# Performance work log

Hardware: AMD Instinct MI355X
Metric: run time of the kernel (lower is better)

The kernel has to match this reference:

```python
import jax, jax.numpy as jnp
import numpy as np


def _gather_nbrs(feats, idx):
    # feats: [C, N], idx: [N, k] -> [C, N, k]
    return feats[:, idx]


def pointconv_dw(xyz, feats, idx, w_pos, b_pos, w_out, b_out):
    """Depthwise point conv: per-channel weights from relative neighbor coords.
    xyz: [B,3,N], feats: [B,C,N], idx: [B,N,k] -> [B,C_out,N]
    """
    nbr_xyz = jax.vmap(_gather_nbrs)(xyz, idx)            # [B,3,N,k]
    rel = nbr_xyz - xyz[:, :, :, None]                    # relative positions
    w = jnp.einsum('cd,bdnk->bcnk', w_pos, rel) + b_pos[None, :, None, None]
    g = jax.vmap(_gather_nbrs)(feats, idx)                # [B,C,N,k]
    agg = jnp.sum(w * g, axis=-1)                         # [B,C,N] depthwise reduce over k
    return jnp.einsum('oc,bcn->bon', w_out, agg) + b_out[None, :, None]


def setup_inputs() -> dict:
    key = jax.random.key(0)
    ks = jax.random.split(key, 16)
    B, N, K = 2, 65536, 4
    IN, HID = 64, 64
    C = HID + IN
    s = 0.02
    inp = {
        'xyz': jax.random.normal(ks[0], (B, 3, N), jnp.float32),
        'h': jax.random.normal(ks[1], (B, HID, N), jnp.float32),
        'x': jax.random.normal(ks[2], (B, IN, N), jnp.float32),
        'knn_indices': jax.random.randint(ks[3], (B, N, K), 0, N, jnp.int32),
    }
    names = ['z', 'r', 'q']
    for i, nm in enumerate(names):
        inp[f'w{nm}_pos'] = s * jax.random.normal(ks[4 + 4 * i], (C, 3), jnp.float32)
        inp[f'b{nm}_pos'] = jnp.zeros((C,), jnp.float32)
        inp[f'w{nm}_out'] = s * jax.random.normal(ks[5 + 4 * i], (HID, C), jnp.float32)
        inp[f'b{nm}_out'] = jnp.zeros((HID,), jnp.float32)
    return inp


def reference(xyz, h, x, knn_indices,
              wz_pos, bz_pos, wz_out, bz_out,
              wr_pos, br_pos, wr_out, br_out,
              wq_pos, bq_pos, wq_out, bq_out):
    hx = jnp.concatenate([h, x], axis=1)                  # [B, HID+IN, N]
    z = jax.nn.sigmoid(pointconv_dw(xyz, hx, knn_indices, wz_pos, bz_pos, wz_out, bz_out))
    r = jax.nn.sigmoid(pointconv_dw(xyz, hx, knn_indices, wr_pos, br_pos, wr_out, br_out))
    rhx = jnp.concatenate([r * h, x], axis=1)
    q = jnp.tanh(pointconv_dw(xyz, rhx, knn_indices, wq_pos, bq_pos, wq_out, bq_out))
    return (1.0 - z) * h + z * q
```

## Files before the change

### kernel.cpp

```cpp
#include <hip/hip_runtime.h>

#define NPTS 65536
#define BATCH 2
#define CCH 128
#define HIDC 64
#define PPB 32
#define LDB 520
#define PLD 136

typedef unsigned short u16;
typedef unsigned int u32;
typedef __bf16 bf16_t;
typedef bf16_t bf16x8 __attribute__((ext_vector_type(8)));
typedef float f32x4 __attribute__((ext_vector_type(4)));

__device__ __forceinline__ u16 f2bf(float f){
  union { float f; unsigned u; } v; v.f = f;
  unsigned r = v.u + 0x7FFFu + ((v.u >> 16) & 1u);
  return (u16)(r >> 16);
}
__device__ __forceinline__ float bf2f(u16 u){
  union { unsigned u; float f; } v; v.u = ((unsigned)u) << 16; return v.f;
}
__device__ __forceinline__ u32 pkrn(float a, float b){
  union { float f; u32 u; } ua, ub; ua.f = a; ub.f = b;
  return ((ua.u + 0x8000u) >> 16) | ((ub.u + 0x8000u) & 0xffff0000u);
}
__device__ __forceinline__ float sigmoidf_(float v){ return 1.f/(1.f+__expf(-v)); }
__device__ __forceinline__ float tanhf_(float v){
  v = fminf(10.f, fmaxf(-10.f, v));
  float e = __expf(2.f*v);
  return (e-1.f)/(e+1.f);
}

__global__ __launch_bounds__(256) void kprep(
    const float* __restrict__ wz, const float* __restrict__ wzp, const float* __restrict__ bzp,
    const float* __restrict__ wr, const float* __restrict__ wrp, const float* __restrict__ brp,
    const float* __restrict__ wq, const float* __restrict__ wqp, const float* __restrict__ bqp,
    u16* __restrict__ A){
  int idx = blockIdx.x*256 + threadIdx.x;
  int t = idx & 7, o = (idx>>3)&63, quad = (idx>>9)&3, s = (idx>>11)&15, g = idx>>15;
  int pk = s*32 + quad*8 + t;
  int j = pk>>7, chunk = (pk>>3)&15, tt = pk&7;
  int orig = chunk*32 + j*8 + tt;
  int c = orig>>2, m = orig&3;
  const float* W  = (g==0)? wz  : (g==1)? wr  : wq;
  const float* wp = (g==0)? wzp : (g==1)? wrp : wqp;
  const float* bp = (g==0)? bzp : (g==1)? brp : bqp;
  float coef = m ? wp[c*3 + m - 1] : bp[c];
  A[idx] = f2bf(W[o*CCH + c] * coef);
}

__global__ __launch_bounds__(256) void k_pack(const float* __restrict__ h,
    const float* __restrict__ x, u16* __restrict__ hxT, u16* __restrict__ rhxT){
  __shared__ __align__(16) u16 tile[64*PLD];
  int tid = threadIdx.x;
  int b = blockIdx.x >> 10, n0 = (blockIdx.x & 1023) << 6;
  #pragma unroll
  for (int i = 0; i < 8; ++i){
    int cc = (tid>>4) + i*16;
    int nn = (tid & 15)*4;
    const float* src = (cc < HIDC)
        ? (h + (((size_t)(b*HIDC + cc))<<16) + n0 + nn)
        : (x + (((size_t)(b*HIDC + cc - HIDC))<<16) + n0 + nn);
    float4 v = *(const float4*)src;
    tile[(nn+0)*PLD + cc] = f2bf(v.x);
    tile[(nn+1)*PLD + cc] = f2bf(v.y);
    tile[(nn+2)*PLD + cc] = f2bf(v.z);
    tile[(nn+3)*PLD + cc] = f2bf(v.w);
  }
  __syncthreads();
  #pragma unroll
  for (int i = 0; i < 4; ++i){
    int tsk = tid + (i<<8);
    int n = tsk>>4, ch = (tsk&15)*8;
    uint4 v = *(const uint4*)(tile + n*PLD + ch);
    *(uint4*)(hxT + (((size_t)(b<<16) + n0 + n)<<7) + ch) = v;
  }
  #pragma unroll
  for (int i = 0; i < 2; ++i){
    int tsk = tid + (i<<8);
    int n = tsk>>3, ch = HIDC + (tsk&7)*8;
    uint4 v = *(const uint4*)(tile + n*PLD + ch);
    *(uint4*)(rhxT + (((size_t)(b<<16) + n0 + n)<<7) + ch) = v;
  }
}

#define ACCUM(gv, rv) { \
  u32 dw_[4] = {gv.x, gv.y, gv.z, gv.w}; \
  _Pragma("unroll") \
  for (int q_ = 0; q_ < 4; ++q_){ \
    union { u32 u; float f; } lo_, hi_; \
    lo_.u = dw_[q_] << 16; hi_.u = dw_[q_] & 0xffff0000u; \
    m0[2*q_]   += lo_.f; mx[2*q_]   += rv.x*lo_.f; my[2*q_]   += rv.y*lo_.f; mz[2*q_]   += rv.z*lo_.f; \
    m0[2*q_+1] += hi_.f; mx[2*q_+1] += rv.x*hi_.f; my[2*q_+1] += rv.y*hi_.f; mz[2*q_+1] += rv.z*hi_.f; \
  } }

__global__ __launch_bounds__(256, 4) void k_zr(
    const float* __restrict__ xyz, const float* __restrict__ h,
    const int* __restrict__ knn,
    const float* __restrict__ bz_out, const float* __restrict__ br_out,
    const u16* __restrict__ Azr,
    const u16* __restrict__ hxT, u16* __restrict__ rhxT, u16* __restrict__ z_ws)
{
  __shared__ __align__(16) u16 bext[PPB*LDB];
  __shared__ __align__(16) float4 relk[PPB*4];
  __shared__ __align__(16) int4 jlds[PPB];

  int tid = threadIdx.x; int lane = tid & 63; int wv = tid >> 6;
  int b = blockIdx.x >> 11, n0 = (blockIdx.x & 2047) << 5;
  size_t bN = (size_t)b * NPTS;

  if (tid < 128){
    int p = tid >> 2, k = tid & 3;
    int j = knn[((bN + n0 + p) << 2) + k];
    ((int*)jlds)[tid] = j;
    const float* xb = xyz + (size_t)b*3*NPTS;
    float cx = xb[n0+p], cy = xb[NPTS + n0+p], cz = xb[2*NPTS + n0+p];
    relk[tid] = make_float4(xb[j]-cx, xb[NPTS+j]-cy, xb[2*NPTS+j]-cz, 0.f);
  }
  __syncthreads();

  const u16* hxTb = hxT + (bN << 7);
  #pragma unroll
  for (int it = 0; it < 2; ++it){
    int task = tid + (it << 8);
    int p = task >> 4, chunk = task & 15;
    int4 jj = jlds[p];
    uint4 g0 = *(const uint4*)(hxTb + (((size_t)jj.x)<<7) + chunk*8);
    uint4 g1 = *(const uint4*)(hxTb + (((size_t)jj.y)<<7) + chunk*8);
    uint4 g2 = *(const uint4*)(hxTb + (((size_t)jj.z)<<7) + chunk*8);
    uint4 g3 = *(const uint4*)(hxTb + (((size_t)jj.w)<<7) + chunk*8);
    float4 r0 = relk[p*4+0], r1 = relk[p*4+1], r2 = relk[p*4+2], r3 = relk[p*4+3];
    float m0[8] = {0,0,0,0,0,0,0,0}, mx[8] = {0,0,0,0,0,0,0,0};
    float my[8] = {0,0,0,0,0,0,0,0}, mz[8] = {0,0,0,0,0,0,0,0};
    ACCUM(g0, r0); ACCUM(g1, r1); ACCUM(g2, r2); ACCUM(g3, r3);
    u16* row = bext + p*LDB;
    #pragma unroll
    for (int j = 0; j < 4; ++j){
      int ca = 2*j, cb = 2*j+1;
      uint4 v;
      v.x = pkrn(m0[ca], mx[ca]); v.y = pkrn(my[ca], mz[ca]);
      v.z = pkrn(m0[cb], mx[cb]); v.w = pkrn(my[cb], mz[cb]);
      *(uint4*)(row + j*128 + chunk*8) = v;
    }
  }
  __syncthreads();

  int l15 = lane & 15, quad = lane >> 4;
  int orow = wv*16 + l15;
  f32x4 accz[2], accr[2];
  #pragma unroll
  for (int nt = 0; nt < 2; ++nt){ accz[nt] = (f32x4){0,0,0,0}; accr[nt] = (f32x4){0,0,0,0}; }
  #pragma unroll
  for (int s = 0; s < 16; ++s){
    bf16x8 az = *(const bf16x8*)(Azr + ((s*4 + quad)*64 + orow)*8);
    bf16x8 ar = *(const bf16x8*)(Azr + 32768 + ((s*4 + quad)*64 + orow)*8);
    #pragma unroll
    for (int nt = 0; nt < 2; ++nt){
      bf16x8 bb = *(const bf16x8*)(bext + (nt*16 + l15)*LDB + s*32 + quad*8);
      accz[nt] = __builtin_amdgcn_mfma_f32_16x16x32_bf16(az, bb, accz[nt], 0, 0, 0);
      accr[nt] = __builtin_amdgcn_mfma_f32_16x16x32_bf16(ar, bb, accr[nt], 0, 0, 0);
    }
  }
  __syncthreads();

  u16* zst  = bext;
  u16* rhst = bext + 64*40;
  #pragma unroll
  for (int nt = 0; nt < 2; ++nt){
    #pragma unroll
    for (int reg = 0; reg < 4; ++reg){
      int o = wv*16 + quad*4 + reg;
      int p = nt*16 + l15;
      float zf = sigmoidf_(accz[nt][reg] + bz_out[o]);
      float rf = sigmoidf_(accr[nt][reg] + br_out[o]);
      float hv = h[(((size_t)(b*HIDC + o))<<16) + n0 + p];
      zst[o*40 + p] = f2bf(zf);
      rhst[p*72 + o] = f2bf(rf * hv);
    }
  }
  __syncthreads();

  {
    int p = tid >> 3, ch = (tid & 7)*8;
    uint4 v = *(const uint4*)(rhst + p*72 + ch);
    *(uint4*)(rhxT + ((bN + n0 + p)<<7) + ch) = v;
  }
  {
    int o = tid >> 2, pc = (tid & 3)*8;
    uint4 v = *(const uint4*)(zst + o*40 + pc);
    *(uint4*)(z_ws + (((size_t)(b*HIDC + o))<<16) + n0 + pc) = v;
  }
}

__global__ __launch_bounds__(256, 4) void k_q(
    const float* __restrict__ xyz, const float* __restrict__ h,
    const int* __restrict__ knn,
    const float* __restrict__ bq_out,
    const u16* __restrict__ Aq,
    const u16* __restrict__ rhxT, const u16* __restrict__ z_ws,
    float* __restrict__ out)
{
  __shared__ __align__(16) u16 bext[PPB*LDB];
  __shared__ __align__(16) float4 relk[PPB*4];
  __shared__ __align__(16) int4 jlds[PPB];

  int tid = threadIdx.x; int lane = tid & 63; int wv = tid >> 6;
  int b = blockIdx.x >> 11, n0 = (blockIdx.x & 2047) << 5;
  size_t bN = (size_t)b * NPTS;

  if (tid < 128){
    int p = tid >> 2, k = tid & 3;
    int j = knn[((bN + n0 + p) << 2) + k];
    ((int*)jlds)[tid] = j;
    const float* xb = xyz + (size_t)b*3*NPTS;
    float cx = xb[n0+p], cy = xb[NPTS + n0+p], cz = xb[2*NPTS + n0+p];
    relk[tid] = make_float4(xb[j]-cx, xb[NPTS+j]-cy, xb[2*NPTS+j]-cz, 0.f);
  }
  __syncthreads();

  const u16* rhxTb = rhxT + (bN << 7);
  #pragma unroll
  for (int it = 0; it < 2; ++it){
    int task = tid + (it << 8);
    int p = task >> 4, chunk = task & 15;
    int4 jj = jlds[p];
    uint4 g0 = *(const uint4*)(rhxTb + (((size_t)jj.x)<<7) + chunk*8);
    uint4 g1 = *(const uint4*)(rhxTb + (((size_t)jj.y)<<7) + chunk*8);
    uint4 g2 = *(const uint4*)(rhxTb + (((size_t)jj.z)<<7) + chunk*8);
    uint4 g3 = *(const uint4*)(rhxTb + (((size_t)jj.w)<<7) + chunk*8);
    float4 r0 = relk[p*4+0], r1 = relk[p*4+1], r2 = relk[p*4+2], r3 = relk[p*4+3];
    float m0[8] = {0,0,0,0,0,0,0,0}, mx[8] = {0,0,0,0,0,0,0,0};
    float my[8] = {0,0,0,0,0,0,0,0}, mz[8] = {0,0,0,0,0,0,0,0};
    ACCUM(g0, r0); ACCUM(g1, r1); ACCUM(g2, r2); ACCUM(g3, r3);
    u16* row = bext + p*LDB;
    #pragma unroll
    for (int j = 0; j < 4; ++j){
      int ca = 2*j, cb = 2*j+1;
      uint4 v;
      v.x = pkrn(m0[ca], mx[ca]); v.y = pkrn(my[ca], mz[ca]);
      v.z = pkrn(m0[cb], mx[cb]); v.w = pkrn(my[cb], mz[cb]);
      *(uint4*)(row + j*128 + chunk*8) = v;
    }
  }
  __syncthreads();

  int l15 = lane & 15, quad = lane >> 4;
  int orow = wv*16 + l15;
  f32x4 acc[2];
  #pragma unroll
  for (int nt = 0; nt < 2; ++nt) acc[nt] = (f32x4){0,0,0,0};
  #pragma unroll
  for (int s = 0; s < 16; ++s){
    bf16x8 aq = *(const bf16x8*)(Aq + ((s*4 + quad)*64 + orow)*8);
    #pragma unroll
    for (int nt = 0; nt < 2; ++nt){
      bf16x8 bb = *(const bf16x8*)(bext + (nt*16 + l15)*LDB + s*32 + quad*8);
      acc[nt] = __builtin_amdgcn_mfma_f32_16x16x32_bf16(aq, bb, acc[nt], 0, 0, 0);
    }
  }

  #pragma unroll
  for (int nt = 0; nt < 2; ++nt){
    #pragma unroll
    for (int reg = 0; reg < 4; ++reg){
      int o = wv*16 + quad*4 + reg;
      int p = nt*16 + l15;
      size_t idx = (((size_t)(b*HIDC + o))<<16) + n0 + p;
      float qf = tanhf_(acc[nt][reg] + bq_out[o]);
      float zf = bf2f(z_ws[idx]);
      float hv = h[idx];
      out[idx] = (1.f - zf)*hv + zf*qf;
    }
  }
}

extern "C" void kernel_launch(void* const* d_in, const int* in_sizes, int n_in,
                              void* d_out, int out_size, void* d_ws, size_t ws_size,
                              hipStream_t stream){
  const float* xyz    = (const float*)d_in[0];
  const float* h      = (const float*)d_in[1];
  const float* x      = (const float*)d_in[2];
  const int*   knn    = (const int*)d_in[3];
  const float* wz_pos = (const float*)d_in[4];
  const float* bz_pos = (const float*)d_in[5];
  const float* wz_out = (const float*)d_in[6];
  const float* bz_out = (const float*)d_in[7];
  const float* wr_pos = (const float*)d_in[8];
  const float* br_pos = (const float*)d_in[9];
  const float* wr_out = (const float*)d_in[10];
  const float* br_out = (const float*)d_in[11];
  const float* wq_pos = (const float*)d_in[12];
  const float* bq_pos = (const float*)d_in[13];
  const float* wq_out = (const float*)d_in[14];
  const float* bq_out = (const float*)d_in[15];
  float* out = (float*)d_out;

  u16* ws   = (u16*)d_ws;
  u16* hxT  = ws;
  u16* rhxT = hxT + (size_t)BATCH*NPTS*CCH;
  u16* z_ws = rhxT + (size_t)BATCH*NPTS*CCH;
  u16* A    = z_ws + (size_t)BATCH*HIDC*NPTS;

  kprep<<<384, 256, 0, stream>>>(wz_out, wz_pos, bz_pos, wr_out, wr_pos, br_pos,
                                 wq_out, wq_pos, bq_pos, A);
  k_pack<<<2048, 256, 0, stream>>>(h, x, hxT, rhxT);
  k_zr<<<4096, 256, 0, stream>>>(xyz, h, knn, bz_out, br_out, A, hxT, rhxT, z_ws);
  k_q<<<4096, 256, 0, stream>>>(xyz, h, knn, bq_out, A + 65536, rhxT, z_ws, out);
}
```

Baseline: 234.9 us.

## Split q conv into x-part computed in k_zr and gather only r*h in k_q

The q pointconv is linear in its input channels, so the contribution from the x channels (which do not depend on r) is computed inside k_zr using the already-gathered hx features and stored as a bf16 pre-activation. k_q then gathers only the 64 r*h channels from a narrower 64-channel buffer and processes 64 points per block. k_pack no longer writes x into a second buffer. This is meant to cut gather traffic and MFMA work in k_q, at the cost of extra MFMAs and an extra output stream in k_zr, plus bf16 rounding of the partial sum.

```diff
diff --git a/kernel.cpp b/kernel.cpp
--- a/kernel.cpp
+++ b/kernel.cpp
@@ -4,9 +4,9 @@
 #define BATCH 2
 #define CCH 128
 #define HIDC 64
-#define PPB 32
 #define LDB 520
-#define PLD 136
+#define LDB2 264
+#define PLD 130
 
 typedef unsigned short u16;
 typedef unsigned int u32;
@@ -39,20 +39,31 @@
     const float* __restrict__ wq, const float* __restrict__ wqp, const float* __restrict__ bqp,
     u16* __restrict__ A){
   int idx = blockIdx.x*256 + threadIdx.x;
-  int t = idx & 7, o = (idx>>3)&63, quad = (idx>>9)&3, s = (idx>>11)&15, g = idx>>15;
-  int pk = s*32 + quad*8 + t;
-  int j = pk>>7, chunk = (pk>>3)&15, tt = pk&7;
-  int orig = chunk*32 + j*8 + tt;
-  int c = orig>>2, m = orig&3;
-  const float* W  = (g==0)? wz  : (g==1)? wr  : wq;
-  const float* wp = (g==0)? wzp : (g==1)? wrp : wqp;
-  const float* bp = (g==0)? bzp : (g==1)? brp : bqp;
-  float coef = m ? wp[c*3 + m - 1] : bp[c];
-  A[idx] = f2bf(W[o*CCH + c] * coef);
+  if (idx < 98304){
+    int t = idx & 7, o = (idx>>3)&63, quad = (idx>>9)&3, s = (idx>>11)&15, g = idx>>15;
+    int pk = s*32 + quad*8 + t;
+    int j = pk>>7, chunk = (pk>>3)&15, tt = pk&7;
+    int orig = chunk*32 + j*8 + tt;
+    int c = orig>>2, m = orig&3;
+    const float* W  = (g==0)? wz  : (g==1)? wr  : wq;
+    const float* wp = (g==0)? wzp : (g==1)? wrp : wqp;
+    const float* bp = (g==0)? bzp : (g==1)? brp : bqp;
+    float coef = m ? wp[c*3 + m - 1] : bp[c];
+    A[idx] = f2bf(W[o*CCH + c] * coef);
+  } else {
+    int i2 = idx - 98304;
+    int t = i2 & 7, o = (i2>>3)&63, quad = (i2>>9)&3, s = (i2>>11)&7;
+    int k2 = s*32 + quad*8 + t;
+    int j = k2>>6, chunk = (k2>>3)&7, tt = k2&7;
+    int orig = chunk*32 + j*8 + tt;
+    int c = orig>>2, m = orig&3;
+    float coef = m ? wqp[c*3 + m - 1] : bqp[c];
+    A[idx] = f2bf(wq[o*CCH + c] * coef);
+  }
 }
 
 __global__ __launch_bounds__(256) void k_pack(const float* __restrict__ h,
-    const float* __restrict__ x, u16* __restrict__ hxT, u16* __restrict__ rhxT){
+    const float* __restrict__ x, u16* __restrict__ hxT){
   __shared__ __align__(16) u16 tile[64*PLD];
   int tid = threadIdx.x;
   int b = blockIdx.x >> 10, n0 = (blockIdx.x & 1023) << 6;
@@ -77,13 +88,6 @@
     uint4 v = *(const uint4*)(tile + n*PLD + ch);
     *(uint4*)(hxT + (((size_t)(b<<16) + n0 + n)<<7) + ch) = v;
   }
-  #pragma unroll
-  for (int i = 0; i < 2; ++i){
-    int tsk = tid + (i<<8);
-    int n = tsk>>3, ch = HIDC + (tsk&7)*8;
-    uint4 v = *(const uint4*)(tile + n*PLD + ch);
-    *(uint4*)(rhxT + (((size_t)(b<<16) + n0 + n)<<7) + ch) = v;
-  }
 }
 
 #define ACCUM(gv, rv) { \
@@ -96,16 +100,27 @@
     m0[2*q_+1] += hi_.f; mx[2*q_+1] += rv.x*hi_.f; my[2*q_+1] += rv.y*hi_.f; mz[2*q_+1] += rv.z*hi_.f; \
   } }
 
+#define PACKROW(row, CHOFF, STRIDE) { \
+  _Pragma("unroll") \
+  for (int j_ = 0; j_ < 4; ++j_){ \
+    int ca_ = 2*j_, cb_ = 2*j_+1; \
+    uint4 v_; \
+    v_.x = pkrn(m0[ca_], mx[ca_]); v_.y = pkrn(my[ca_], mz[ca_]); \
+    v_.z = pkrn(m0[cb_], mx[cb_]); v_.w = pkrn(my[cb_], mz[cb_]); \
+    *(uint4*)((row) + j_*(STRIDE) + (CHOFF)) = v_; \
+  } }
+
 __global__ __launch_bounds__(256, 4) void k_zr(
     const float* __restrict__ xyz, const float* __restrict__ h,
     const int* __restrict__ knn,
     const float* __restrict__ bz_out, const float* __restrict__ br_out,
     const u16* __restrict__ Azr,
-    const u16* __restrict__ hxT, u16* __restrict__ rhxT, u16* __restrict__ z_ws)
+    const u16* __restrict__ hxT, u16* __restrict__ rhT,
+    u16* __restrict__ z_ws, u16* __restrict__ qx_ws)
 {
-  __shared__ __align__(16) u16 bext[PPB*LDB];
-  __shared__ __align__(16) float4 relk[PPB*4];
-  __shared__ __align__(16) int4 jlds[PPB];
+  __shared__ __align__(16) u16 bext[32*LDB];
+  __shared__ __align__(16) float4 relk[128];
+  __shared__ __align__(16) int4 jlds[32];
 
   int tid = threadIdx.x; int lane = tid & 63; int wv = tid >> 6;
   int b = blockIdx.x >> 11, n0 = (blockIdx.x & 2047) << 5;
@@ -122,51 +137,68 @@
   __syncthreads();
 
   const u16* hxTb = hxT + (bN << 7);
-  #pragma unroll
-  for (int it = 0; it < 2; ++it){
-    int task = tid + (it << 8);
-    int p = task >> 4, chunk = task & 15;
-    int4 jj = jlds[p];
-    uint4 g0 = *(const uint4*)(hxTb + (((size_t)jj.x)<<7) + chunk*8);
-    uint4 g1 = *(const uint4*)(hxTb + (((size_t)jj.y)<<7) + chunk*8);
-    uint4 g2 = *(const uint4*)(hxTb + (((size_t)jj.z)<<7) + chunk*8);
-    uint4 g3 = *(const uint4*)(hxTb + (((size_t)jj.w)<<7) + chunk*8);
-    float4 r0 = relk[p*4+0], r1 = relk[p*4+1], r2 = relk[p*4+2], r3 = relk[p*4+3];
+  int pA = tid >> 4, chk = tid & 15;
+  int pB = pA + 16;
+  int4 jA = jlds[pA], jB = jlds[pB];
+  const u16* cb = hxTb + chk*8;
+  uint4 ga0 = *(const uint4*)(cb + (((size_t)jA.x)<<7));
+  uint4 ga1 = *(const uint4*)(cb + (((size_t)jA.y)<<7));
+  uint4 ga2 = *(const uint4*)(cb + (((size_t)jA.z)<<7));
+  uint4 ga3 = *(const uint4*)(cb + (((size_t)jA.w)<<7));
+  uint4 gb0 = *(const uint4*)(cb + (((size_t)jB.x)<<7));
+  uint4 gb1 = *(const uint4*)(cb + (((size_t)jB.y)<<7));
+  uint4 gb2 = *(const uint4*)(cb + (((size_t)jB.z)<<7));
+  uint4 gb3 = *(const uint4*)(cb + (((size_t)jB.w)<<7));
+  {
+    float4 r0 = relk[pA*4+0], r1 = relk[pA*4+1], r2 = relk[pA*4+2], r3 = relk[pA*4+3];
     float m0[8] = {0,0,0,0,0,0,0,0}, mx[8] = {0,0,0,0,0,0,0,0};
     float my[8] = {0,0,0,0,0,0,0,0}, mz[8] = {0,0,0,0,0,0,0,0};
-    ACCUM(g0, r0); ACCUM(g1, r1); ACCUM(g2, r2); ACCUM(g3, r3);
-    u16* row = bext + p*LDB;
-    #pragma unroll
-    for (int j = 0; j < 4; ++j){
-      int ca = 2*j, cb = 2*j+1;
-      uint4 v;
-      v.x = pkrn(m0[ca], mx[ca]); v.y = pkrn(my[ca], mz[ca]);
-      v.z = pkrn(m0[cb], mx[cb]); v.w = pkrn(my[cb], mz[cb]);
-      *(uint4*)(row + j*128 + chunk*8) = v;
-    }
+    ACCUM(ga0, r0); ACCUM(ga1, r1); ACCUM(ga2, r2); ACCUM(ga3, r3);
+    PACKROW(bext + pA*LDB, chk*8, 128);
+  }
+  {
+    float4 r0 = relk[pB*4+0], r1 = relk[pB*4+1], r2 = relk[pB*4+2], r3 = relk[pB*4+3];
+    float m0[8] = {0,0,0,0,0,0,0,0}, mx[8] = {0,0,0,0,0,0,0,0};
+    float my[8] = {0,0,0,0,0,0,0,0}, mz[8] = {0,0,0,0,0,0,0,0};
+    ACCUM(gb0, r0); ACCUM(gb1, r1); ACCUM(gb2, r2); ACCUM(gb3, r3);
+    PACKROW(bext + pB*LDB, chk*8, 128);
   }
   __syncthreads();
 
   int l15 = lane & 15, quad = lane >> 4;
   int orow = wv*16 + l15;
-  f32x4 accz[2], accr[2];
-  #pragma unroll
-  for (int nt = 0; nt < 2; ++nt){ accz[nt] = (f32x4){0,0,0,0}; accr[nt] = (f32x4){0,0,0,0}; }
+  f32x4 accz[2], accr[2], accq[2];
+  #pragma unroll
+  for (int nt = 0; nt < 2; ++nt){
+    accz[nt] = (f32x4){0,0,0,0}; accr[nt] = (f32x4){0,0,0,0}; accq[nt] = (f32x4){0,0,0,0};
+  }
   #pragma unroll
   for (int s = 0; s < 16; ++s){
     bf16x8 az = *(const bf16x8*)(Azr + ((s*4 + quad)*64 + orow)*8);
     bf16x8 ar = *(const bf16x8*)(Azr + 32768 + ((s*4 + quad)*64 + orow)*8);
-    #pragma unroll
-    for (int nt = 0; nt < 2; ++nt){
-      bf16x8 bb = *(const bf16x8*)(bext + (nt*16 + l15)*LDB + s*32 + quad*8);
-      accz[nt] = __builtin_amdgcn_mfma_f32_16x16x32_bf16(az, bb, accz[nt], 0, 0, 0);
-      accr[nt] = __builtin_amdgcn_mfma_f32_16x16x32_bf16(ar, bb, accr[nt], 0, 0, 0);
+    if (s & 2){
+      bf16x8 aq = *(const bf16x8*)(Azr + 65536 + ((s*4 + quad)*64 + orow)*8);
+      #pragma unroll
+      for (int nt = 0; nt < 2; ++nt){
+        bf16x8 bb = *(const bf16x8*)(bext + (nt*16 + l15)*LDB + s*32 + quad*8);
+        accz[nt] = __builtin_amdgcn_mfma_f32_16x16x32_bf16(az, bb, accz[nt], 0, 0, 0);
+        accr[nt] = __builtin_amdgcn_mfma_f32_16x16x32_bf16(ar, bb, accr[nt], 0, 0, 0);
+        accq[nt] = __builtin_amdgcn_mfma_f32_16x16x32_bf16(aq, bb, accq[nt], 0, 0, 0);
+      }
+    } else {
+      #pragma unroll
+      for (int nt = 0; nt < 2; ++nt){
+        bf16x8 bb = *(const bf16x8*)(bext + (nt*16 + l15)*LDB + s*32 + quad*8);
+        accz[nt] = __builtin_amdgcn_mfma_f32_16x16x32_bf16(az, bb, accz[nt], 0, 0, 0);
+        accr[nt] = __builtin_amdgcn_mfma_f32_16x16x32_bf16(ar, bb, accr[nt], 0, 0, 0);
+      }
     }
   }
   __syncthreads();
 
   u16* zst  = bext;
-  u16* rhst = bext + 64*40;
+  u16* rhst = bext + 2560;
+  u16* qxst = bext + 2560 + 2304;
   #pragma unroll
   for (int nt = 0; nt < 2; ++nt){
     #pragma unroll
@@ -178,6 +210,7 @@
       float hv = h[(((size_t)(b*HIDC + o))<<16) + n0 + p];
       zst[o*40 + p] = f2bf(zf);
       rhst[p*72 + o] = f2bf(rf * hv);
+      qxst[o*40 + p] = f2bf(accq[nt][reg]);
     }
   }
   __syncthreads();
@@ -185,12 +218,17 @@
   {
     int p = tid >> 3, ch = (tid & 7)*8;
     uint4 v = *(const uint4*)(rhst + p*72 + ch);
-    *(uint4*)(rhxT + ((bN + n0 + p)<<7) + ch) = v;
+    *(uint4*)(rhT + ((bN + n0 + p)<<6) + ch) = v;
   }
   {
     int o = tid >> 2, pc = (tid & 3)*8;
     uint4 v = *(const uint4*)(zst + o*40 + pc);
     *(uint4*)(z_ws + (((size_t)(b*HIDC + o))<<16) + n0 + pc) = v;
+  }
+  {
+    int o = tid >> 2, pc = (tid & 3)*8;
+    uint4 v = *(const uint4*)(qxst + o*40 + pc);
+    *(uint4*)(qx_ws + (((size_t)(b*HIDC + o))<<16) + n0 + pc) = v;
   }
 }
 
@@ -198,19 +236,19 @@
     const float* __restrict__ xyz, const float* __restrict__ h,
     const int* __restrict__ knn,
     const float* __restrict__ bq_out,
-    const u16* __restrict__ Aq,
-    const u16* __restrict__ rhxT, const u16* __restrict__ z_ws,
-    float* __restrict__ out)
+    const u16* __restrict__ Aqrh,
+    const u16* __restrict__ rhT, const u16* __restrict__ z_ws,
+    const u16* __restrict__ qx_ws, float* __restrict__ out)
 {
-  __shared__ __align__(16) u16 bext[PPB*LDB];
-  __shared__ __align__(16) float4 relk[PPB*4];
-  __shared__ __align__(16) int4 jlds[PPB];
+  __shared__ __align__(16) u16 bext[64*LDB2];
+  __shared__ __align__(16) float4 relk[256];
+  __shared__ __align__(16) int4 jlds[64];
 
   int tid = threadIdx.x; int lane = tid & 63; int wv = tid >> 6;
-  int b = blockIdx.x >> 11, n0 = (blockIdx.x & 2047) << 5;
+  int b = blockIdx.x >> 10, n0 = (blockIdx.x & 1023) << 6;
   size_t bN = (size_t)b * NPTS;
 
-  if (tid < 128){
+  {
     int p = tid >> 2, k = tid & 3;
     int j = knn[((bN + n0 + p) << 2) + k];
     ((int*)jlds)[tid] = j;
@@ -220,55 +258,59 @@
   }
   __syncthreads();
 
-  const u16* rhxTb = rhxT + (bN << 7);
-  #pragma unroll
-  for (int it = 0; it < 2; ++it){
-    int task = tid + (it << 8);
-    int p = task >> 4, chunk = task & 15;
-    int4 jj = jlds[p];
-    uint4 g0 = *(const uint4*)(rhxTb + (((size_t)jj.x)<<7) + chunk*8);
-    uint4 g1 = *(const uint4*)(rhxTb + (((size_t)jj.y)<<7) + chunk*8);
-    uint4 g2 = *(const uint4*)(rhxTb + (((size_t)jj.z)<<7) + chunk*8);
-    uint4 g3 = *(const uint4*)(rhxTb + (((size_t)jj.w)<<7) + chunk*8);
-    float4 r0 = relk[p*4+0], r1 = relk[p*4+1], r2 = relk[p*4+2], r3 = relk[p*4+3];
+  const u16* rhTb = rhT + (bN << 6);
+  int pA = tid >> 3, chk = tid & 7;
+  int pB = pA + 32;
+  int4 jA = jlds[pA], jB = jlds[pB];
+  const u16* cb = rhTb + chk*8;
+  uint4 ga0 = *(const uint4*)(cb + (((size_t)jA.x)<<6));
+  uint4 ga1 = *(const uint4*)(cb + (((size_t)jA.y)<<6));
+  uint4 ga2 = *(const uint4*)(cb + (((size_t)jA.z)<<6));
+  uint4 ga3 = *(const uint4*)(cb + (((size_t)jA.w)<<6));
+  uint4 gb0 = *(const uint4*)(cb + (((size_t)jB.x)<<6));
+  uint4 gb1 = *(const uint4*)(cb + (((size_t)jB.y)<<6));
+  uint4 gb2 = *(const uint4*)(cb + (((size_t)jB.z)<<6));
+  uint4 gb3 = *(const uint4*)(cb + (((size_t)jB.w)<<6));
+  {
+    float4 r0 = relk[pA*4+0], r1 = relk[pA*4+1], r2 = relk[pA*4+2], r3 = relk[pA*4+3];
     float m0[8] = {0,0,0,0,0,0,0,0}, mx[8] = {0,0,0,0,0,0,0,0};
     float my[8] = {0,0,0,0,0,0,0,0}, mz[8] = {0,0,0,0,0,0,0,0};
-    ACCUM(g0, r0); ACCUM(g1, r1); ACCUM(g2, r2); ACCUM(g3, r3);
-    u16* row = bext + p*LDB;
-    #pragma unroll
-    for (int j = 0; j < 4; ++j){
-      int ca = 2*j, cb = 2*j+1;
-      uint4 v;
-      v.x = pkrn(m0[ca], mx[ca]); v.y = pkrn(my[ca], mz[ca]);
-      v.z = pkrn(m0[cb], mx[cb]); v.w = pkrn(my[cb], mz[cb]);
-      *(uint4*)(row + j*128 + chunk*8) = v;
-    }
+    ACCUM(ga0, r0); ACCUM(ga1, r1); ACCUM(ga2, r2); ACCUM(ga3, r3);
+    PACKROW(bext + pA*LDB2, chk*8, 64);
+  }
+  {
+    float4 r0 = relk[pB*4+0], r1 = relk[pB*4+1], r2 = relk[pB*4+2], r3 = relk[pB*4+3];
+    float m0[8] = {0,0,0,0,0,0,0,0}, mx[8] = {0,0,0,0,0,0,0,0};
+    float my[8] = {0,0,0,0,0,0,0,0}, mz[8] = {0,0,0,0,0,0,0,0};
+    ACCUM(gb0, r0); ACCUM(gb1, r1); ACCUM(gb2, r2); ACCUM(gb3, r3);
+    PACKROW(bext + pB*LDB2, chk*8, 64);
   }
   __syncthreads();
 
   int l15 = lane & 15, quad = lane >> 4;
   int orow = wv*16 + l15;
-  f32x4 acc[2];
-  #pragma unroll
-  for (int nt = 0; nt < 2; ++nt) acc[nt] = (f32x4){0,0,0,0};
-  #pragma unroll
-  for (int s = 0; s < 16; ++s){
-    bf16x8 aq = *(const bf16x8*)(Aq + ((s*4 + quad)*64 + orow)*8);
+  f32x4 acc[4];
+  #pragma unroll
+  for (int nt = 0; nt < 4; ++nt) acc[nt] = (f32x4){0,0,0,0};
+  #pragma unroll
+  for (int s = 0; s < 8; ++s){
+    bf16x8 aq = *(const bf16x8*)(Aqrh + ((s*4 + quad)*64 + orow)*8);
     #pragma unroll
-    for (int nt = 0; nt < 2; ++nt){
-      bf16x8 bb = *(const bf16x8*)(bext + (nt*16 + l15)*LDB + s*32 + quad*8);
+    for (int nt = 0; nt < 4; ++nt){
+      bf16x8 bb = *(const bf16x8*)(bext + (nt*16 + l15)*LDB2 + s*32 + quad*8);
       acc[nt] = __builtin_amdgcn_mfma_f32_16x16x32_bf16(aq, bb, acc[nt], 0, 0, 0);
     }
   }
 
   #pragma unroll
-  for (int nt = 0; nt < 2; ++nt){
+  for (int nt = 0; nt < 4; ++nt){
     #pragma unroll
     for (int reg = 0; reg < 4; ++reg){
       int o = wv*16 + quad*4 + reg;
       int p = nt*16 + l15;
       size_t idx = (((size_t)(b*HIDC + o))<<16) + n0 + p;
-      float qf = tanhf_(acc[nt][reg] + bq_out[o]);
+      float qpre = acc[nt][reg] + bq_out[o] + bf2f(qx_ws[idx]);
+      float qf = tanhf_(qpre);
       float zf = bf2f(z_ws[idx]);
       float hv = h[idx];
       out[idx] = (1.f - zf)*hv + zf*qf;
@@ -297,15 +339,16 @@
   const float* bq_out = (const float*)d_in[15];
   float* out = (float*)d_out;
 
-  u16* ws   = (u16*)d_ws;
-  u16* hxT  = ws;
-  u16* rhxT = hxT + (size_t)BATCH*NPTS*CCH;
-  u16* z_ws = rhxT + (size_t)BATCH*NPTS*CCH;
-  u16* A    = z_ws + (size_t)BATCH*HIDC*NPTS;
-
-  kprep<<<384, 256, 0, stream>>>(wz_out, wz_pos, bz_pos, wr_out, wr_pos, br_pos,
+  u16* ws    = (u16*)d_ws;
+  u16* hxT   = ws;
+  u16* rhT   = ws + 16777216;
+  u16* z_ws  = ws + 25165824;
+  u16* qx_ws = ws + 33554432;
+  u16* A     = ws + 41943040;
+
+  kprep<<<448, 256, 0, stream>>>(wz_out, wz_pos, bz_pos, wr_out, wr_pos, br_pos,
                                  wq_out, wq_pos, bq_pos, A);
-  k_pack<<<2048, 256, 0, stream>>>(h, x, hxT, rhxT);
-  k_zr<<<4096, 256, 0, stream>>>(xyz, h, knn, bz_out, br_out, A, hxT, rhxT, z_ws);
-  k_q<<<4096, 256, 0, stream>>>(xyz, h, knn, bq_out, A + 65536, rhxT, z_ws, out);
-}
+  k_pack<<<2048, 256, 0, stream>>>(h, x, hxT);
+  k_zr<<<4096, 256, 0, stream>>>(xyz, h, knn, bz_out, br_out, A, hxT, rhT, z_ws, qx_ws);
+  k_q<<<2048, 256, 0, stream>>>(xyz, h, knn, bq_out, A + 98304, rhT, z_ws, qx_ws, out);
+}
```

Result: faster. 222.5 us (-5.3%).
